# Performance work log

Measured on AMD Instinct MI355X. Metric: run time of the kernel, lower is better.

Reference implementation:

```python
import jax, jax.numpy as jnp
import numpy as np


def setup_inputs() -> dict:
    key = jax.random.key(0)
    ks = jax.random.split(key, 6)
    B, Cx, Cf, Ch, H, W = 4, 512, 512, 256, 64, 64
    return {
        "query_features": jax.random.normal(ks[0], (B, Cx, H, W), dtype=jnp.float32),
        "reference_features": jax.random.normal(ks[1], (B, Cf, H, W), dtype=jnp.float32),
        "Wq": jax.random.normal(ks[2], (Ch, Cx), dtype=jnp.float32) * (1.0 / np.sqrt(Cx)),
        "bq": jax.random.normal(ks[3], (Ch,), dtype=jnp.float32) * 0.02,
        "Wk": jax.random.normal(ks[4], (Ch, Cf), dtype=jnp.float32) * (1.0 / np.sqrt(Cf)),
        "bk": jax.random.normal(ks[5], (Ch,), dtype=jnp.float32) * 0.02,
    }


def reference(query_features, reference_features, Wq, bq, Wk, bk):
    # 1x1 convs == per-pixel linear projections over channels
    Q = jnp.einsum('bchw,oc->bohw', query_features, Wq) + bq[None, :, None, None]
    K = jnp.einsum('bchw,oc->bohw', reference_features, Wk) + bk[None, :, None, None]
    B, Cf, H2, W2 = reference_features.shape
    H1, W1 = Q.shape[2], Q.shape[3]
    V = reference_features.reshape(B, Cf, H2 * W2)            # b c p
    # unscaled QK^T over hidden channels: [b, h1, w1, h2*w2]
    scores = jnp.einsum('bcij,bckl->bijkl', Q, K).reshape(B, H1, W1, H2 * W2)
    attn = jax.nn.softmax(scores, axis=-1)
    out = jnp.einsum('bijp,bcp->bcij', attn, V)               # [b, Cf, h1, w1]
    return out
```

## Files before the change

kernel.cpp:

```cpp
#include <hip/hip_runtime.h>
#include <hip/hip_bf16.h>
#include <hip/hip_fp16.h>

typedef _Float16 half8 __attribute__((ext_vector_type(8)));
typedef _Float16 half4v __attribute__((ext_vector_type(4)));
typedef float f4 __attribute__((ext_vector_type(4)));
typedef float f16v __attribute__((ext_vector_type(16)));
typedef short short8 __attribute__((ext_vector_type(8)));
typedef unsigned short us8 __attribute__((ext_vector_type(8)));
typedef int i4 __attribute__((ext_vector_type(4)));

#define P_SZ 4096
#define CH 256
#define CIN 512
#define CV 512
#define KVB 32
#define L2E 1.4426950408889634f

__device__ __forceinline__ unsigned short f2bf(float f) {
  unsigned u = __float_as_uint(f);
  unsigned r = u + 0x7fffu + ((u >> 16) & 1u);
  return (unsigned short)(r >> 16);
}
__device__ __forceinline__ float bf2f(unsigned short h) {
  return __uint_as_float(((unsigned)h) << 16);
}

__device__ __forceinline__ void gload16(const void* g, void* l) {
  __builtin_amdgcn_global_load_lds(
      (const __attribute__((address_space(1))) unsigned int*)g,
      (__attribute__((address_space(3))) unsigned int*)l, 16, 0, 0);
}

__global__ __launch_bounds__(256) void wconv_kernel(
    const float* __restrict__ Wq, const float* __restrict__ Wk,
    short* __restrict__ Wh, short* __restrict__ Wl) {
  const int i = blockIdx.x * 256 + threadIdx.x;
  const int which = i >> 17;
  const int j = i & 131071;
  const float w = which ? Wk[j] : Wq[j] * L2E;
  const unsigned short h = f2bf(w);
  Wh[i] = (short)h;
  Wl[i] = (short)f2bf(w - bf2f(h));
}

__global__ __launch_bounds__(256) void vconv_kernel(const float* __restrict__ in,
                                                    _Float16* __restrict__ outv) {
  const size_t i = (size_t)blockIdx.x * 256 + threadIdx.x;
  const f4 x = ((const f4*)in)[i];
  half4v h;
  h[0] = (_Float16)x[0]; h[1] = (_Float16)x[1];
  h[2] = (_Float16)x[2]; h[3] = (_Float16)x[3];
  const int pq = (int)(i & 1023);
  const int ch = (int)((i >> 10) & 511);
  const int b  = (int)(i >> 19);
  const int p0 = pq * 4;
  const size_t idx = (size_t)b * 2097152 + (size_t)(p0 >> 5) * 16384
                   + (size_t)((p0 >> 3) & 3) * 4096 + ch * 8 + (p0 & 7);
  *(half4v*)(outv + idx) = h;
}

__global__ __launch_bounds__(512) void proj_kernel(
    const float* __restrict__ Xq, const float* __restrict__ bq,
    const float* __restrict__ Xk, const float* __restrict__ bk,
    const short* __restrict__ Wh, const short* __restrict__ Wl,
    _Float16* __restrict__ Qout, _Float16* __restrict__ Kout) {
  const int which = blockIdx.z;
  const float* __restrict__ X = which ? Xk : Xq;
  const float* __restrict__ bias = which ? bk : bq;
  _Float16* __restrict__ out = which ? Kout : Qout;
  const float bscale = which ? 1.f : L2E;

  const int b = blockIdx.y;
  const int p0 = blockIdx.x * 64;
  const int tid = threadIdx.x;
  const int w = tid >> 6, l = tid & 63;
  const int wp = w >> 2, wo = w & 3;
  const int lr = l & 15, lg = l >> 4;

  const float* __restrict__ Xb = X + (size_t)b * CIN * P_SZ;
  const short* __restrict__ Whb = Wh + (size_t)which * 131072;
  const short* __restrict__ Wlb = Wl + (size_t)which * 131072;

  f4 acc[2][4];
  #pragma unroll
  for (int m = 0; m < 2; ++m)
    #pragma unroll
    for (int n = 0; n < 4; ++n) acc[m][n] = (f4){0.f, 0.f, 0.f, 0.f};

  const int prow0 = p0 + wp * 32 + lr;

  #pragma unroll 1
  for (int kc = 0; kc < CIN; kc += 32) {
    short8 ah[2], al[2];
    #pragma unroll
    for (int m = 0; m < 2; ++m) {
      const float* xp = Xb + (size_t)(kc + lg * 8) * P_SZ + (prow0 + m * 16);
      #pragma unroll
      for (int i = 0; i < 8; ++i) {
        float xv = xp[(size_t)i * P_SZ];
        unsigned short h = f2bf(xv);
        ah[m][i] = (short)h;
        al[m][i] = (short)f2bf(xv - bf2f(h));
      }
    }
    short8 bh[4], bl[4];
    #pragma unroll
    for (int n = 0; n < 4; ++n) {
      const size_t wi = (size_t)(wo * 64 + n * 16 + lr) * CIN + kc + lg * 8;
      bh[n] = *(const short8*)(Whb + wi);
      bl[n] = *(const short8*)(Wlb + wi);
    }
    #pragma unroll
    for (int m = 0; m < 2; ++m)
      #pragma unroll
      for (int n = 0; n < 4; ++n) {
        acc[m][n] = __builtin_amdgcn_mfma_f32_16x16x32_bf16(ah[m], bh[n], acc[m][n], 0, 0, 0);
        acc[m][n] = __builtin_amdgcn_mfma_f32_16x16x32_bf16(ah[m], bl[n], acc[m][n], 0, 0, 0);
        acc[m][n] = __builtin_amdgcn_mfma_f32_16x16x32_bf16(al[m], bh[n], acc[m][n], 0, 0, 0);
      }
  }

  #pragma unroll
  for (int n = 0; n < 4; ++n) {
    const int o = wo * 64 + n * 16 + lr;
    const float bv = bias[o] * bscale;
    #pragma unroll
    for (int m = 0; m < 2; ++m) {
      #pragma unroll
      for (int j = 0; j < 4; ++j) {
        const int p = p0 + wp * 32 + m * 16 + lg * 4 + j;
        const _Float16 val = (_Float16)(acc[m][n][j] + bv);
        if (which == 0) {
          out[((size_t)b * P_SZ + p) * CH + o] = val;
        } else {
          const int kk = p & 31;
          const int kswz = (kk & 19) | ((kk & 4) << 1) | ((kk & 8) >> 1);
          out[(size_t)b * 1048576 + (size_t)(p >> 5) * 8192
              + (size_t)(o >> 3) * 256 + kswz * 8 + (o & 7)] = val;
        }
      }
    }
  }
}

template <int NSEG, bool DIRECT>
__global__ __launch_bounds__(512, 2) void attn_kernel(
    const _Float16* __restrict__ Qg, const _Float16* __restrict__ Kt,
    const _Float16* __restrict__ Vt, unsigned short* __restrict__ Opart,
    float* __restrict__ Mp, float* __restrict__ Lp, float* __restrict__ Og) {
  __shared__ char K_l[3][16384];
  __shared__ char V_l[3][32768];

  constexpr int nt = (P_SZ / NSEG) / KVB;
  int b, qt, seg;
  if (NSEG == 2) {
    const int g = blockIdx.x & 7;
    b = g >> 1; seg = g & 1; qt = blockIdx.x >> 3;
  } else {
    b = blockIdx.x & 3; seg = 0; qt = blockIdx.x >> 2;
  }

  const int tid = threadIdx.x;
  const int w = tid >> 6, l = tid & 63;
  const int hi = l >> 5, l31 = l & 31;
  const int wq = w >> 1, half = w & 1;

  const char* Kb = (const char*)Kt + (size_t)b * 2097152 + (size_t)seg * nt * 16384;
  const char* Vb = (const char*)Vt + (size_t)b * 4194304 + (size_t)seg * nt * 32768;

#define STAGE(BUF, T) do { \
    const char* ksrc = Kb + (size_t)(T) * 16384; \
    const char* vsrc = Vb + (size_t)(T) * 32768; \
    gload16(ksrc + tid * 16,         &K_l[BUF][w * 1024]); \
    gload16(ksrc + 8192 + tid * 16,  &K_l[BUF][8192 + w * 1024]); \
    gload16(vsrc + tid * 16,         &V_l[BUF][w * 1024]); \
    gload16(vsrc + 8192 + tid * 16,  &V_l[BUF][8192 + w * 1024]); \
    gload16(vsrc + 16384 + tid * 16, &V_l[BUF][16384 + w * 1024]); \
    gload16(vsrc + 24576 + tid * 16, &V_l[BUF][24576 + w * 1024]); \
  } while (0)

  half8 qf[16];
  {
    const char* qrow = (const char*)Qg +
        ((size_t)b * P_SZ + qt * 128 + wq * 32 + l31) * 512;
    #pragma unroll
    for (int m = 0; m < 16; ++m) qf[m] = *(const half8*)(qrow + m * 32 + hi * 16);
  }

  f16v acc[8];
  #pragma unroll
  for (int n = 0; n < 8; ++n)
    acc[n] = (f16v){0,0,0,0, 0,0,0,0, 0,0,0,0, 0,0,0,0};

  float m_run = -1e30f, lsum = 0.f;
  const int kread = hi * 512 + l31 * 16;
  const int vread = hi * 8192 + half * 4096 + l31 * 16;

  STAGE(0, 0); STAGE(1, 1);
  asm volatile("s_waitcnt vmcnt(6)" ::: "memory");
  asm volatile("s_barrier" ::: "memory");
  __builtin_amdgcn_sched_barrier(0);

  int bufc = 0;
  #pragma unroll 1
  for (int t = 0; t < nt; ++t) {
    const char* kb = &K_l[bufc][0] + kread;
    f16v s = (f16v){0,0,0,0, 0,0,0,0, 0,0,0,0, 0,0,0,0};
    __builtin_amdgcn_s_setprio(1);
    #pragma unroll
    for (int m = 0; m < 16; ++m) {
      half8 kf = *(const half8*)(kb + m * 1024);
      s = __builtin_amdgcn_mfma_f32_32x32x16_f16(kf, qf[m], s, 0, 0, 0);
    }
    __builtin_amdgcn_s_setprio(0);

    float x0 = fmaxf(s[0], s[8]),  x1 = fmaxf(s[1], s[9]);
    float x2 = fmaxf(s[2], s[10]), x3 = fmaxf(s[3], s[11]);
    float x4 = fmaxf(s[4], s[12]), x5 = fmaxf(s[5], s[13]);
    float x6 = fmaxf(s[6], s[14]), x7 = fmaxf(s[7], s[15]);
    x0 = fmaxf(x0, x4); x1 = fmaxf(x1, x5); x2 = fmaxf(x2, x6); x3 = fmaxf(x3, x7);
    float pm = fmaxf(fmaxf(x0, x1), fmaxf(x2, x3));
    pm = fmaxf(pm, __shfl_xor(pm, 32));
    if (__any(pm > m_run + 12.f)) {
      const float mnew = fmaxf(m_run, pm);
      const float al = __builtin_amdgcn_exp2f(m_run - mnew);
      const int alb = __float_as_int(al);
      #pragma unroll
      for (int r = 0; r < 16; ++r) {
        const int cr = (r & 3) + 8 * (r >> 2);
        const float ar = __int_as_float(
            __builtin_amdgcn_ds_bpermute(cr * 4 + hi * 16, alb));
        #pragma unroll
        for (int n = 0; n < 8; ++n) acc[n][r] *= ar;
      }
      lsum *= al;
      m_run = mnew;
    }
    float p[16], psum;
    #pragma unroll
    for (int r = 0; r < 16; ++r) p[r] = __builtin_amdgcn_exp2f(s[r] - m_run);
    {
      float a0 = (p[0] + p[1]) + (p[2] + p[3]);
      float a1 = (p[4] + p[5]) + (p[6] + p[7]);
      float a2 = (p[8] + p[9]) + (p[10] + p[11]);
      float a3 = (p[12] + p[13]) + (p[14] + p[15]);
      psum = (a0 + a1) + (a2 + a3);
      psum += __shfl_xor(psum, 32);
    }
    lsum += psum;

    i4 w0v, w1v;
    w0v[0] = __builtin_bit_cast(int, __builtin_amdgcn_cvt_pkrtz(p[0], p[1]));
    w0v[1] = __builtin_bit_cast(int, __builtin_amdgcn_cvt_pkrtz(p[2], p[3]));
    w0v[2] = __builtin_bit_cast(int, __builtin_amdgcn_cvt_pkrtz(p[4], p[5]));
    w0v[3] = __builtin_bit_cast(int, __builtin_amdgcn_cvt_pkrtz(p[6], p[7]));
    w1v[0] = __builtin_bit_cast(int, __builtin_amdgcn_cvt_pkrtz(p[8], p[9]));
    w1v[1] = __builtin_bit_cast(int, __builtin_amdgcn_cvt_pkrtz(p[10], p[11]));
    w1v[2] = __builtin_bit_cast(int, __builtin_amdgcn_cvt_pkrtz(p[12], p[13]));
    w1v[3] = __builtin_bit_cast(int, __builtin_amdgcn_cvt_pkrtz(p[14], p[15]));
    const half8 pa0 = __builtin_bit_cast(half8, w0v);
    const half8 pa1 = __builtin_bit_cast(half8, w1v);

    const int bufs = bufc == 0 ? 2 : bufc - 1;
    if (t + 2 < nt) STAGE(bufs, t + 2);

    const char* vb = &V_l[bufc][0] + vread;
    __builtin_amdgcn_s_setprio(1);
    #pragma unroll
    for (int n = 0; n < 8; ++n) {
      half8 v0 = *(const half8*)(vb + n * 512);
      acc[n] = __builtin_amdgcn_mfma_f32_32x32x16_f16(pa0, v0, acc[n], 0, 0, 0);
      half8 v1 = *(const half8*)(vb + 16384 + n * 512);
      acc[n] = __builtin_amdgcn_mfma_f32_32x32x16_f16(pa1, v1, acc[n], 0, 0, 0);
    }
    __builtin_amdgcn_s_setprio(0);

    if (t + 2 < nt) { asm volatile("s_waitcnt vmcnt(6)" ::: "memory"); }
    else            { asm volatile("s_waitcnt vmcnt(0)" ::: "memory"); }
    asm volatile("s_barrier" ::: "memory");
    __builtin_amdgcn_sched_barrier(0);
    bufc = bufc == 2 ? 0 : bufc + 1;
  }
#undef STAGE

  const int qg0 = qt * 128 + wq * 32;
  if (!DIRECT) {
    unsigned short* Ob = Opart +
        (((size_t)seg * 4 + b) * P_SZ + qg0) * 512 + half * 256 + l31;
    #pragma unroll
    for (int n = 0; n < 8; ++n) {
      #pragma unroll
      for (int r = 0; r < 16; ++r) {
        const int q = (r & 3) + 8 * (r >> 2) + 4 * hi;
        Ob[(size_t)q * 512 + n * 32] = f2bf(acc[n][r]);
      }
    }
    if (half == 0 && l < 32) {
      const size_t mi = ((size_t)seg * 4 + b) * P_SZ + qg0 + l31;
      Mp[mi] = m_run; Lp[mi] = lsum;
    }
  } else {
    float linv[16];
    const int lb = __float_as_int(lsum);
    #pragma unroll
    for (int r = 0; r < 16; ++r) {
      const int cr = (r & 3) + 8 * (r >> 2);
      const float lq = __int_as_float(__builtin_amdgcn_ds_bpermute(cr * 4 + hi * 16, lb));
      linv[r] = 1.f / lq;
    }
    #pragma unroll
    for (int n = 0; n < 8; ++n) {
      #pragma unroll
      for (int r = 0; r < 16; ++r) {
        const int q = (r & 3) + 8 * (r >> 2) + 4 * hi;
        Og[((size_t)b * CV + half * 256 + n * 32 + l31) * P_SZ + qg0 + q] =
            acc[n][r] * linv[r];
      }
    }
  }
}

template <int NSEG>
__global__ __launch_bounds__(256) void combine_kernel(
    const unsigned short* __restrict__ Opart, const float* __restrict__ Mp,
    const float* __restrict__ Lp, float* __restrict__ Og) {
  __shared__ float T[64][65];
  const int bx = blockIdx.x;
  const int ct = bx & 7, qt = (bx >> 3) & 63, b = bx >> 9;
  const int tid = threadIdx.x;
  {
    const int qi = tid >> 2, cj = tid & 3;
    const int q = qt * 64 + qi;
    const size_t mibase = (size_t)b * P_SZ + q;
    float M = -1e30f;
    #pragma unroll
    for (int s = 0; s < NSEG; ++s) M = fmaxf(M, Mp[(size_t)s * 4 * P_SZ + mibase]);
    float L = 0.f;
    float o[16];
    #pragma unroll
    for (int e = 0; e < 16; ++e) o[e] = 0.f;
    #pragma unroll
    for (int s = 0; s < NSEG; ++s) {
      const float wgt = __builtin_amdgcn_exp2f(Mp[(size_t)s * 4 * P_SZ + mibase] - M);
      L += wgt * Lp[(size_t)s * 4 * P_SZ + mibase];
      const unsigned short* src = Opart +
          (((size_t)s * 4 + b) * P_SZ + q) * 512 + ct * 64 + cj * 16;
      const us8 ua = ((const us8*)src)[0];
      const us8 ub = ((const us8*)src)[1];
      #pragma unroll
      for (int e = 0; e < 8; ++e) {
        o[e]     += wgt * bf2f(ua[e]);
        o[8 + e] += wgt * bf2f(ub[e]);
      }
    }
    const float inv = 1.f / L;
    #pragma unroll
    for (int e = 0; e < 16; ++e) T[qi][cj * 16 + e] = o[e] * inv;
  }
  __syncthreads();
  const int ci = tid >> 2, qj = tid & 3;
  #pragma unroll
  for (int i = 0; i < 4; ++i) {
    f4 v;
    #pragma unroll
    for (int e = 0; e < 4; ++e) v[e] = T[qj * 16 + i * 4 + e][ci];
    *(f4*)&Og[((size_t)b * CV + ct * 64 + ci) * P_SZ + qt * 64 + qj * 16 + i * 4] = v;
  }
}

extern "C" void kernel_launch(void* const* d_in, const int* in_sizes, int n_in,
                              void* d_out, int out_size, void* d_ws, size_t ws_size,
                              hipStream_t stream) {
  const float* x  = (const float*)d_in[0];
  const float* f  = (const float*)d_in[1];
  const float* Wq = (const float*)d_in[2];
  const float* bq = (const float*)d_in[3];
  const float* Wk = (const float*)d_in[4];
  const float* bk = (const float*)d_in[5];
  float* out = (float*)d_out;

  char* ws = (char*)d_ws;
  _Float16* Qf = (_Float16*)ws;
  _Float16* Kf = (_Float16*)(ws + ((size_t)8 << 20));
  _Float16* Vf = (_Float16*)(ws + ((size_t)16 << 20));
  float* Mp    = (float*)(ws + ((size_t)32 << 20));
  float* Lp    = (float*)(ws + ((size_t)32 << 20) + (256 << 10));
  short* Wh    = (short*)(ws + ((size_t)32 << 20) + (512 << 10));
  short* Wl    = (short*)(ws + ((size_t)33 << 20));
  unsigned short* Opart = (unsigned short*)(ws + ((size_t)34 << 20));

  wconv_kernel<<<dim3(1024), dim3(256), 0, stream>>>(Wq, Wk, Wh, Wl);
  vconv_kernel<<<dim3(8192), dim3(256), 0, stream>>>(f, Vf);
  proj_kernel<<<dim3(64, 4, 2), dim3(512), 0, stream>>>(x, bq, f, bk, Wh, Wl, Qf, Kf);

  const size_t need2 = ((size_t)34 << 20) + ((size_t)32 << 20);
  const size_t need1 = ((size_t)34 << 20) + ((size_t)16 << 20);
  if (ws_size >= need2) {
    attn_kernel<2, false><<<dim3(256), dim3(512), 0, stream>>>(Qf, Kf, Vf, Opart, Mp, Lp, nullptr);
    combine_kernel<2><<<dim3(2048), dim3(256), 0, stream>>>(Opart, Mp, Lp, out);
  } else if (ws_size >= need1) {
    attn_kernel<1, false><<<dim3(128), dim3(512), 0, stream>>>(Qf, Kf, Vf, Opart, Mp, Lp, nullptr);
    combine_kernel<1><<<dim3(2048), dim3(256), 0, stream>>>(Opart, Mp, Lp, out);
  } else {
    attn_kernel<1, true><<<dim3(128), dim3(512), 0, stream>>>(Qf, Kf, Vf, nullptr, nullptr, nullptr, out);
  }
}
```

Baseline: 261.5 us.

## Transpose V conversion through shared memory and split QK MFMA chain

The V fp32-to-fp16 conversion kernel now stages a 512-channel by 32-pixel tile in LDS, so its global stores become contiguous 16-byte writes instead of scattered 8-byte writes. It uses 512 blocks instead of 8192. Separately, the QK^T score loop in the attention kernel splits its single dependent 16-step MFMA accumulation into two independent chains that are summed at the end, to hide MFMA latency. The cost is an extra vector add and more accumulator registers, which could reduce occupancy, plus fewer blocks in the conversion kernel.

```diff
diff --git a/kernel.cpp b/kernel.cpp
--- a/kernel.cpp
+++ b/kernel.cpp
@@ -46,18 +46,29 @@
 
 __global__ __launch_bounds__(256) void vconv_kernel(const float* __restrict__ in,
                                                     _Float16* __restrict__ outv) {
-  const size_t i = (size_t)blockIdx.x * 256 + threadIdx.x;
-  const f4 x = ((const f4*)in)[i];
-  half4v h;
-  h[0] = (_Float16)x[0]; h[1] = (_Float16)x[1];
-  h[2] = (_Float16)x[2]; h[3] = (_Float16)x[3];
-  const int pq = (int)(i & 1023);
-  const int ch = (int)((i >> 10) & 511);
-  const int b  = (int)(i >> 19);
-  const int p0 = pq * 4;
-  const size_t idx = (size_t)b * 2097152 + (size_t)(p0 >> 5) * 16384
-                   + (size_t)((p0 >> 3) & 3) * 4096 + ch * 8 + (p0 & 7);
-  *(half4v*)(outv + idx) = h;
+  __shared__ _Float16 T[512][34];
+  const int b = blockIdx.x >> 7;
+  const int tile = blockIdx.x & 127;
+  const int tid = threadIdx.x;
+  const float* src = in + (size_t)b * CIN * P_SZ + tile * 32;
+  const int c0 = tid >> 3, j4 = tid & 7;
+  #pragma unroll
+  for (int pass = 0; pass < 16; ++pass) {
+    const int c = pass * 32 + c0;
+    const f4 x = *(const f4*)(src + (size_t)c * P_SZ + j4 * 4);
+    half4v h;
+    h[0] = (_Float16)x[0]; h[1] = (_Float16)x[1];
+    h[2] = (_Float16)x[2]; h[3] = (_Float16)x[3];
+    *(half4v*)&T[c][j4 * 4] = h;
+  }
+  __syncthreads();
+  _Float16* dst = outv + (size_t)b * 2097152 + (size_t)tile * 16384;
+  #pragma unroll
+  for (int i = 0; i < 8; ++i) {
+    const int kh = i >> 1;
+    const int ch = ((i & 1) << 8) + tid;
+    *(half8*)(dst + kh * 4096 + ch * 8) = *(const half8*)&T[ch][kh * 8];
+  }
 }
 
 __global__ __launch_bounds__(512) void proj_kernel(
@@ -206,14 +217,18 @@
   #pragma unroll 1
   for (int t = 0; t < nt; ++t) {
     const char* kb = &K_l[bufc][0] + kread;
-    f16v s = (f16v){0,0,0,0, 0,0,0,0, 0,0,0,0, 0,0,0,0};
+    f16v s0_ = (f16v){0,0,0,0, 0,0,0,0, 0,0,0,0, 0,0,0,0};
+    f16v s1_ = (f16v){0,0,0,0, 0,0,0,0, 0,0,0,0, 0,0,0,0};
     __builtin_amdgcn_s_setprio(1);
     #pragma unroll
-    for (int m = 0; m < 16; ++m) {
-      half8 kf = *(const half8*)(kb + m * 1024);
-      s = __builtin_amdgcn_mfma_f32_32x32x16_f16(kf, qf[m], s, 0, 0, 0);
+    for (int m = 0; m < 8; ++m) {
+      half8 kf0 = *(const half8*)(kb + m * 1024);
+      half8 kf1 = *(const half8*)(kb + (m + 8) * 1024);
+      s0_ = __builtin_amdgcn_mfma_f32_32x32x16_f16(kf0, qf[m], s0_, 0, 0, 0);
+      s1_ = __builtin_amdgcn_mfma_f32_32x32x16_f16(kf1, qf[m + 8], s1_, 0, 0, 0);
     }
     __builtin_amdgcn_s_setprio(0);
+    const f16v s = s0_ + s1_;
 
     float x0 = fmaxf(s[0], s[8]),  x1 = fmaxf(s[1], s[9]);
     float x2 = fmaxf(s[2], s[10]), x3 = fmaxf(s[3], s[11]);
@@ -391,7 +406,7 @@
   unsigned short* Opart = (unsigned short*)(ws + ((size_t)34 << 20));
 
   wconv_kernel<<<dim3(1024), dim3(256), 0, stream>>>(Wq, Wk, Wh, Wl);
-  vconv_kernel<<<dim3(8192), dim3(256), 0, stream>>>(f, Vf);
+  vconv_kernel<<<dim3(512), dim3(256), 0, stream>>>(f, Vf);
   proj_kernel<<<dim3(64, 4, 2), dim3(512), 0, stream>>>(x, bq, f, bk, Wh, Wl, Qf, Kf);
 
   const size_t need2 = ((size_t)34 << 20) + ((size_t)32 << 20);
```

New measurement: 257.7 us. About the same (-1.5%).
